# Kernel optimization log

Hardware: AMD Instinct MI355X
Metric: run time of the kernel (lower is better)

Reference implementation:

```python
import jax, jax.numpy as jnp
import numpy as np

B, S, D_IN, D_OUT = 4, 2048, 4096, 11008


def setup_inputs() -> dict:
    key = jax.random.key(0)
    k1, k2, k3, k4 = jax.random.split(key, 4)
    x = jax.random.normal(k1, (B, S, D_IN), dtype=jnp.float32)
    # quantized int8 codes (stored int32 per harness dtype set)
    weight_q = jax.random.randint(k2, (D_OUT, D_IN), 0, 127, dtype=jnp.int32)
    scale = jax.random.uniform(k3, (1,), dtype=jnp.float32) * 0.01 + 1e-4
    bias = jax.random.normal(k4, (D_OUT,), dtype=jnp.float32)
    return {"x": x, "weight_q": weight_q, "scale": scale, "bias": bias}


def reference(x, weight_q, scale, bias):
    # dequantize: int codes * per-tensor scale -> fp32 weight [D_OUT, D_IN]
    weight_fp = weight_q.astype(jnp.float32) * scale[0]
    # F.linear: y = x @ W^T + b
    return jnp.einsum('bsd,od->bso', x, weight_fp) + bias
```

## Files before the change

### kernel.cpp

```cpp
#include <hip/hip_runtime.h>
#include <hip/hip_bf16.h>
#include <stdint.h>

#define M_TOT 8192
#define N_TOT 11008
#define K_TOT 4096
#define BM 256
#define BN 256
#define BK 64
#define KT (K_TOT / BK)
#define NTM (M_TOT / BM)
#define NTN (N_TOT / BN)
#define NBLK (NTM * NTN)
#define BUFB 32768
#define LDSB (4 * BUFB)
#define ROWB K_TOT

typedef int i32x4 __attribute__((ext_vector_type(4)));

__global__ __launch_bounds__(256) void quant_x_kernel(const float* __restrict__ x,
                                                      char* __restrict__ xq,
                                                      float* __restrict__ sr) {
  __shared__ float red[4];
  const int r = blockIdx.x;
  const int t = threadIdx.x;
  const float4* px = (const float4*)(x + (long)r * K_TOT) + t * 4;
  float4 v0 = px[0], v1 = px[1], v2 = px[2], v3 = px[3];
  float f[16] = {v0.x, v0.y, v0.z, v0.w, v1.x, v1.y, v1.z, v1.w,
                 v2.x, v2.y, v2.z, v2.w, v3.x, v3.y, v3.z, v3.w};
  float m = 0.f;
#pragma unroll
  for (int i = 0; i < 16; ++i) m = fmaxf(m, fabsf(f[i]));
#pragma unroll
  for (int off = 1; off < 64; off <<= 1) m = fmaxf(m, __shfl_xor(m, off));
  if ((t & 63) == 0) red[t >> 6] = m;
  __syncthreads();
  m = fmaxf(fmaxf(red[0], red[1]), fmaxf(red[2], red[3]));
  m = fmaxf(m, 1e-20f);
  const float inv = 127.0f / m;
  int q[16];
#pragma unroll
  for (int i = 0; i < 16; ++i) q[i] = __float2int_rn(f[i] * inv);
  int4 o;
  o.x = (q[0] & 255) | ((q[1] & 255) << 8) | ((q[2] & 255) << 16) | (q[3] << 24);
  o.y = (q[4] & 255) | ((q[5] & 255) << 8) | ((q[6] & 255) << 16) | (q[7] << 24);
  o.z = (q[8] & 255) | ((q[9] & 255) << 8) | ((q[10] & 255) << 16) | (q[11] << 24);
  o.w = (q[12] & 255) | ((q[13] & 255) << 8) | ((q[14] & 255) << 16) | (q[15] << 24);
  ((int4*)(xq + (long)r * K_TOT))[t] = o;
  if (t == 0) sr[r] = m / 127.0f;
}

__global__ __launch_bounds__(256) void cvt_w8_kernel(const int* __restrict__ w,
                                                     char* __restrict__ wq,
                                                     long n16) {
  long i = (long)blockIdx.x * 256 + threadIdx.x;
  if (i >= n16) return;
  const int4* p = (const int4*)w + i * 4;
  int4 a = p[0], b = p[1], c = p[2], d = p[3];
  int4 o;
  o.x = (a.x & 255) | ((a.y & 255) << 8) | ((a.z & 255) << 16) | (a.w << 24);
  o.y = (b.x & 255) | ((b.y & 255) << 8) | ((b.z & 255) << 16) | (b.w << 24);
  o.z = (c.x & 255) | ((c.y & 255) << 8) | ((c.z & 255) << 16) | (c.w << 24);
  o.w = (d.x & 255) | ((d.y & 255) << 8) | ((d.z & 255) << 16) | (d.w << 24);
  ((int4*)wq)[i] = o;
}

__device__ __forceinline__ void gload_lds16(const void* g, void* l) {
  __builtin_amdgcn_global_load_lds((const __attribute__((address_space(1))) void*)g,
                                   (__attribute__((address_space(3))) void*)l,
                                   16, 0, 0);
}

__global__ __launch_bounds__(512, 2) void gemm256_i8_kernel(
    const unsigned char* __restrict__ A,
    const unsigned char* __restrict__ Bw,
    const float* __restrict__ sr,
    const float* __restrict__ scale,
    const float* __restrict__ bias,
    float* __restrict__ C) {
  extern __shared__ char lds[];
  const int tid = threadIdx.x;
  const int lane = tid & 63;
  const int wid = tid >> 6;
  const int wm = wid >> 2;
  const int wn = wid & 3;
  const int l16 = lane & 15;
  const int kh = lane >> 4;

  const int bid = blockIdx.x;
  const int wg = (bid & 7) * (NBLK / 8) + (bid >> 3);
  const int tm = wg / NTN, tn = wg % NTN;
  const long m0 = (long)tm * BM, n0 = (long)tn * BN;

  const int prl = tid >> 3;
  const int cp = ((tid & 7) * 16) ^ ((prl & 7) << 4);
  const int hsel = cp >> 6;
  const int colb = cp & 63;
  const char* gA = (const char*)A + (m0 + 2 * prl + hsel) * (long)ROWB + colb;
  const char* gB = (const char*)Bw + (n0 + 2 * prl + hsel) * (long)ROWB + colb;
  const int ldsT = tid * 16;

  const int inner = (((lane & 1) << 6) | (kh << 4)) ^ (((l16 >> 1) & 7) << 4);
  const int aB = (wm * 64 + (l16 >> 1)) * 128 + inner;
  const int bB = 16384 + (wn * 32 + (l16 >> 1)) * 128 + inner;

  i32x4 acc[8][4] = {};
  i32x4 afP[4], afN[4], bfA[4], bfB[4];

#define STG_A(q, kb) gload_lds16(gA + (q) * (128L * ROWB) + (kb), lds + sOff + (q) * 8192 + ldsT)
#define STG_B(q, kb) gload_lds16(gB + (q) * (128L * ROWB) + (kb), lds + sOff + 16384 + (q) * 8192 + ldsT)

  int sOff = 0;
  STG_A(0, 0); STG_A(1, 0); STG_B(0, 0); STG_B(1, 0);
  sOff = BUFB;
  STG_A(0, 64); STG_A(1, 64); STG_B(0, 64); STG_B(1, 64);
  sOff = 2 * BUFB;
  STG_A(0, 128); STG_A(1, 128); STG_B(0, 128); STG_B(1, 128);
  asm volatile("s_waitcnt vmcnt(8)" ::: "memory");
  asm volatile("s_barrier" ::: "memory");
#pragma unroll
  for (int i = 0; i < 4; ++i) {
    afP[i] = *(const i32x4*)(lds + aB + i * 1024);
    bfA[i] = *(const i32x4*)(lds + bB + i * 1024);
  }

  int cOff = 0;
  sOff = 3 * BUFB;
  long ktB = 3 * 64;
  int t = 0;

#define ITER(BF_CUR, BF_NXT)                                                  \
  {                                                                           \
    const char* La = lds + cOff;                                              \
    if (t < KT - 2) asm volatile("s_waitcnt vmcnt(4)" ::: "memory");          \
    else            asm volatile("s_waitcnt vmcnt(0)" ::: "memory");          \
    asm volatile("s_barrier" ::: "memory");                                   \
    if (t < KT - 3) { STG_A(0, ktB); STG_A(1, ktB); STG_B(0, ktB); STG_B(1, ktB); } \
    _Pragma("unroll")                                                         \
    for (int i = 0; i < 4; ++i)                                               \
      afN[i] = *(const i32x4*)(La + aB + 4096 + i * 1024);                    \
    __builtin_amdgcn_sched_barrier(0);                                        \
    __builtin_amdgcn_s_setprio(1);                                            \
    _Pragma("unroll")                                                         \
    for (int mi = 0; mi < 4; ++mi)                                            \
      _Pragma("unroll")                                                       \
      for (int ni = 0; ni < 4; ++ni)                                          \
        acc[mi][ni] = __builtin_amdgcn_mfma_i32_16x16x64_i8(afP[mi], BF_CUR[ni], acc[mi][ni], 0, 0, 0); \
    __builtin_amdgcn_s_setprio(0);                                            \
    __builtin_amdgcn_sched_barrier(0);                                        \
    if (t < KT - 1) {                                                         \
      const char* Ln = lds + ((cOff + BUFB) & (LDSB - 1));                    \
      _Pragma("unroll")                                                       \
      for (int i = 0; i < 4; ++i) {                                           \
        afP[i] = *(const i32x4*)(Ln + aB + i * 1024);                         \
        BF_NXT[i] = *(const i32x4*)(Ln + bB + i * 1024);                      \
      }                                                                       \
    }                                                                         \
    __builtin_amdgcn_sched_barrier(0);                                        \
    __builtin_amdgcn_s_setprio(1);                                            \
    _Pragma("unroll")                                                         \
    for (int mi = 0; mi < 4; ++mi)                                            \
      _Pragma("unroll")                                                       \
      for (int ni = 0; ni < 4; ++ni)                                          \
        acc[4 + mi][ni] = __builtin_amdgcn_mfma_i32_16x16x64_i8(afN[mi], BF_CUR[ni], acc[4 + mi][ni], 0, 0, 0); \
    __builtin_amdgcn_s_setprio(0);                                            \
    cOff = (cOff + BUFB) & (LDSB - 1);                                        \
    sOff = (sOff + BUFB) & (LDSB - 1);                                        \
    ktB += 64;                                                                \
    ++t;                                                                      \
  }

  for (int tt = 0; tt < KT / 2; ++tt) {
    ITER(bfA, bfB);
    ITER(bfB, bfA);
  }
#undef ITER
#undef STG_A
#undef STG_B

  const float sw = scale[0];
  float bv[4];
#pragma unroll
  for (int ni = 0; ni < 4; ++ni) bv[ni] = bias[n0 + wn * 64 + ni * 16 + l16];
#pragma unroll
  for (int mi = 0; mi < 8; ++mi) {
#pragma unroll
    for (int j = 0; j < 4; ++j) {
      const long row = m0 + wm * 128 + mi * 16 + kh * 4 + j;
      const float rsw = sr[row] * sw;
#pragma unroll
      for (int ni = 0; ni < 4; ++ni) {
        const long col = n0 + wn * 64 + ni * 16 + l16;
        C[row * N_TOT + col] = (float)acc[mi][ni][j] * rsw + bv[ni];
      }
    }
  }
}

__global__ __launch_bounds__(256) void naive_kernel(const float* __restrict__ x,
                                                    const int* __restrict__ wq,
                                                    const float* __restrict__ scale,
                                                    const float* __restrict__ bias,
                                                    float* __restrict__ out) {
  long idx = (long)blockIdx.x * 256 + threadIdx.x;
  if (idx >= (long)M_TOT * N_TOT) return;
  long m = idx / N_TOT, n = idx % N_TOT;
  const float* xr = x + m * (long)K_TOT;
  const int* wr = wq + n * (long)K_TOT;
  float acc = 0.f;
  for (int k = 0; k < K_TOT; ++k) acc += xr[k] * (float)wr[k];
  out[idx] = acc * scale[0] + bias[n];
}

extern "C" void kernel_launch(void* const* d_in, const int* in_sizes, int n_in,
                              void* d_out, int out_size, void* d_ws, size_t ws_size,
                              hipStream_t stream) {
  const float* x = (const float*)d_in[0];
  const int* wq = (const int*)d_in[1];
  const float* scale = (const float*)d_in[2];
  const float* bias = (const float*)d_in[3];
  float* out = (float*)d_out;

  const long xe = (long)M_TOT * K_TOT;
  const long we = (long)N_TOT * K_TOT;
  const size_t need = (size_t)xe + we + M_TOT * sizeof(float);

  if (ws_size >= need) {
    char* xq = (char*)d_ws;
    char* wb = xq + xe;
    float* sr = (float*)(wb + we);
    quant_x_kernel<<<M_TOT, 256, 0, stream>>>(x, xq, sr);
    cvt_w8_kernel<<<(int)((we / 16 + 255) / 256), 256, 0, stream>>>(wq, wb, we / 16);
    (void)hipFuncSetAttribute((const void*)gemm256_i8_kernel,
                              hipFuncAttributeMaxDynamicSharedMemorySize, LDSB);
    gemm256_i8_kernel<<<NBLK, 512, LDSB, stream>>>((const unsigned char*)xq,
                                                   (const unsigned char*)wb,
                                                   sr, scale, bias, out);
  } else {
    long total = (long)M_TOT * N_TOT;
    naive_kernel<<<(int)((total + 255) / 256), 256, 0, stream>>>(x, wq, scale, bias, out);
  }
}
```

Baseline: 463.2 us.

## Load A operand directly from global into registers, stage only B in LDS

The A tile no longer passes through LDS. Each wave now loads its A fragments straight from global memory into registers with inline global_load_dwordx4, and only the B tile is staged in LDS, which halves the LDS buffer size. This is meant to cut LDS traffic and LDS footprint, possibly allowing better occupancy. The cost is more global loads per wave and a more fragile vmcnt-based wait scheme, and the direct A loads may coalesce poorly and miss the reuse that LDS sharing across waves provided.

```diff
diff --git a/kernel.cpp b/kernel.cpp
--- a/kernel.cpp
+++ b/kernel.cpp
@@ -12,7 +12,7 @@
 #define NTM (M_TOT / BM)
 #define NTN (N_TOT / BN)
 #define NBLK (NTM * NTN)
-#define BUFB 32768
+#define BUFB 16384
 #define LDSB (4 * BUFB)
 #define ROWB K_TOT
 
@@ -70,6 +70,9 @@
                                    (__attribute__((address_space(3))) void*)l,
                                    16, 0, 0);
 }
+
+#define LDG(dst, p) \
+  asm volatile("global_load_dwordx4 %0, %1, off" : "=v"(dst) : "v"((const void*)(p)))
 
 __global__ __launch_bounds__(512, 2) void gemm256_i8_kernel(
     const unsigned char* __restrict__ A,
@@ -96,86 +99,86 @@
   const int cp = ((tid & 7) * 16) ^ ((prl & 7) << 4);
   const int hsel = cp >> 6;
   const int colb = cp & 63;
-  const char* gA = (const char*)A + (m0 + 2 * prl + hsel) * (long)ROWB + colb;
   const char* gB = (const char*)Bw + (n0 + 2 * prl + hsel) * (long)ROWB + colb;
   const int ldsT = tid * 16;
 
   const int inner = (((lane & 1) << 6) | (kh << 4)) ^ (((l16 >> 1) & 7) << 4);
-  const int aB = (wm * 64 + (l16 >> 1)) * 128 + inner;
-  const int bB = 16384 + (wn * 32 + (l16 >> 1)) * 128 + inner;
+  const int bB = (wn * 32 + (l16 >> 1)) * 128 + inner;
+
+  const char* aP = (const char*)A + (m0 + wm * 128 + l16) * (long)ROWB + kh * 16;
 
   i32x4 acc[8][4] = {};
-  i32x4 afP[4], afN[4], bfA[4], bfB[4];
-
-#define STG_A(q, kb) gload_lds16(gA + (q) * (128L * ROWB) + (kb), lds + sOff + (q) * 8192 + ldsT)
-#define STG_B(q, kb) gload_lds16(gB + (q) * (128L * ROWB) + (kb), lds + sOff + 16384 + (q) * 8192 + ldsT)
+  i32x4 aL0[4], aL1[4], aHi[4], bf[4];
+
+#define STG_B(q, kb) gload_lds16(gB + (q) * (128L * ROWB) + (kb), lds + sOff + (q) * 8192 + ldsT)
 
   int sOff = 0;
-  STG_A(0, 0); STG_A(1, 0); STG_B(0, 0); STG_B(1, 0);
+  STG_B(0, 0); STG_B(1, 0);
   sOff = BUFB;
-  STG_A(0, 64); STG_A(1, 64); STG_B(0, 64); STG_B(1, 64);
+  STG_B(0, 64); STG_B(1, 64);
   sOff = 2 * BUFB;
-  STG_A(0, 128); STG_A(1, 128); STG_B(0, 128); STG_B(1, 128);
-  asm volatile("s_waitcnt vmcnt(8)" ::: "memory");
+  STG_B(0, 128); STG_B(1, 128);
+#pragma unroll
+  for (int i = 0; i < 4; ++i) LDG(aL0[i], aP + i * (16L * ROWB));
+  __builtin_amdgcn_sched_barrier(0);
+  asm volatile("s_waitcnt vmcnt(0)" ::: "memory");
+  __builtin_amdgcn_sched_barrier(0);
   asm volatile("s_barrier" ::: "memory");
-#pragma unroll
-  for (int i = 0; i < 4; ++i) {
-    afP[i] = *(const i32x4*)(lds + aB + i * 1024);
-    bfA[i] = *(const i32x4*)(lds + bB + i * 1024);
-  }
 
   int cOff = 0;
   sOff = 3 * BUFB;
+  long ktA = 0;
   long ktB = 3 * 64;
   int t = 0;
 
-#define ITER(BF_CUR, BF_NXT)                                                  \
+#define ITER(ALC, ALN)                                                        \
   {                                                                           \
-    const char* La = lds + cOff;                                              \
-    if (t < KT - 2) asm volatile("s_waitcnt vmcnt(4)" ::: "memory");          \
+    asm volatile("s_barrier" ::: "memory");                 \
+    _Pragma("unroll")                                                         \
+    for (int ni = 0; ni < 4; ++ni)                                            \
+      bf[ni] = *(const i32x4*)(lds + cOff + bB + ni * 1024);                  \
+    _Pragma("unroll")                                                         \
+    for (int i = 0; i < 4; ++i) LDG(aHi[i], aP + (4 + i) * (16L * ROWB) + ktA); \
+    if (t < KT - 1) {                                                         \
+      _Pragma("unroll")                                                       \
+      for (int i = 0; i < 4; ++i) LDG(ALN[i], aP + i * (16L * ROWB) + ktA + 64); \
+    }                                                                         \
+    if (t < KT - 3) { STG_B(0, ktB); STG_B(1, ktB); }                         \
+    __builtin_amdgcn_sched_barrier(0);                                        \
+    if (t < KT - 3) asm volatile("s_waitcnt vmcnt(12)" ::: "memory");         \
     else            asm volatile("s_waitcnt vmcnt(0)" ::: "memory");          \
-    asm volatile("s_barrier" ::: "memory");                                   \
-    if (t < KT - 3) { STG_A(0, ktB); STG_A(1, ktB); STG_B(0, ktB); STG_B(1, ktB); } \
-    _Pragma("unroll")                                                         \
-    for (int i = 0; i < 4; ++i)                                               \
-      afN[i] = *(const i32x4*)(La + aB + 4096 + i * 1024);                    \
     __builtin_amdgcn_sched_barrier(0);                                        \
     __builtin_amdgcn_s_setprio(1);                                            \
     _Pragma("unroll")                                                         \
     for (int mi = 0; mi < 4; ++mi)                                            \
       _Pragma("unroll")                                                       \
       for (int ni = 0; ni < 4; ++ni)                                          \
-        acc[mi][ni] = __builtin_amdgcn_mfma_i32_16x16x64_i8(afP[mi], BF_CUR[ni], acc[mi][ni], 0, 0, 0); \
+        acc[mi][ni] = __builtin_amdgcn_mfma_i32_16x16x64_i8(ALC[mi], bf[ni], acc[mi][ni], 0, 0, 0); \
     __builtin_amdgcn_s_setprio(0);                                            \
     __builtin_amdgcn_sched_barrier(0);                                        \
-    if (t < KT - 1) {                                                         \
-      const char* Ln = lds + ((cOff + BUFB) & (LDSB - 1));                    \
-      _Pragma("unroll")                                                       \
-      for (int i = 0; i < 4; ++i) {                                           \
-        afP[i] = *(const i32x4*)(Ln + aB + i * 1024);                         \
-        BF_NXT[i] = *(const i32x4*)(Ln + bB + i * 1024);                      \
-      }                                                                       \
-    }                                                                         \
+    if (t < KT - 3) asm volatile("s_waitcnt vmcnt(6)" ::: "memory");          \
+    else            asm volatile("s_waitcnt vmcnt(0)" ::: "memory");          \
     __builtin_amdgcn_sched_barrier(0);                                        \
     __builtin_amdgcn_s_setprio(1);                                            \
     _Pragma("unroll")                                                         \
     for (int mi = 0; mi < 4; ++mi)                                            \
       _Pragma("unroll")                                                       \
       for (int ni = 0; ni < 4; ++ni)                                          \
-        acc[4 + mi][ni] = __builtin_amdgcn_mfma_i32_16x16x64_i8(afN[mi], BF_CUR[ni], acc[4 + mi][ni], 0, 0, 0); \
+        acc[4 + mi][ni] = __builtin_amdgcn_mfma_i32_16x16x64_i8(aHi[mi], bf[ni], acc[4 + mi][ni], 0, 0, 0); \
     __builtin_amdgcn_s_setprio(0);                                            \
+    __builtin_amdgcn_sched_barrier(0);                                        \
     cOff = (cOff + BUFB) & (LDSB - 1);                                        \
     sOff = (sOff + BUFB) & (LDSB - 1);                                        \
+    ktA += 64;                                                                \
     ktB += 64;                                                                \
     ++t;                                                                      \
   }
 
   for (int tt = 0; tt < KT / 2; ++tt) {
-    ITER(bfA, bfB);
-    ITER(bfB, bfA);
+    ITER(aL0, aL1);
+    ITER(aL1, aL0);
   }
 #undef ITER
-#undef STG_A
 #undef STG_B
 
   const float sw = scale[0];
```

Result: slower. 913.6 us (+97.2%).

## Shrink GEMM tile to 256x128 with four waves and a three-stage LDS ring

Applied to the files above, without the earlier changes.

The int8 GEMM block tile goes from 256x256 with 8 waves to 256x128 with 4 waves, so each wave keeps its 128x64 accumulator footprint. The LDS ring goes from four stages to three, with stage indices fixed at compile time through a 6-way unrolled loop. The wait and barrier now sit between the two MFMA halves instead of at the top of each iteration. This doubles the block count for better balance across CUs, but reloads more operand data per output, prefetches one stage less, and halves waves resident per CU.

```diff
diff --git a/kernel.cpp b/kernel.cpp
--- a/kernel.cpp
+++ b/kernel.cpp
@@ -6,14 +6,14 @@
 #define N_TOT 11008
 #define K_TOT 4096
 #define BM 256
-#define BN 256
+#define BN 128
 #define BK 64
 #define KT (K_TOT / BK)
 #define NTM (M_TOT / BM)
 #define NTN (N_TOT / BN)
 #define NBLK (NTM * NTN)
-#define BUFB 32768
-#define LDSB (4 * BUFB)
+#define BUFB 24576
+#define LDSB (3 * BUFB)
 #define ROWB K_TOT
 
 typedef int i32x4 __attribute__((ext_vector_type(4)));
@@ -71,7 +71,7 @@
                                    16, 0, 0);
 }
 
-__global__ __launch_bounds__(512, 2) void gemm256_i8_kernel(
+__global__ __launch_bounds__(256, 2) void gemm256_i8_kernel(
     const unsigned char* __restrict__ A,
     const unsigned char* __restrict__ Bw,
     const float* __restrict__ sr,
@@ -82,8 +82,8 @@
   const int tid = threadIdx.x;
   const int lane = tid & 63;
   const int wid = tid >> 6;
-  const int wm = wid >> 2;
-  const int wn = wid & 3;
+  const int wm = wid >> 1;
+  const int wn = wid & 1;
   const int l16 = lane & 15;
   const int kh = lane >> 4;
 
@@ -107,16 +107,16 @@
   i32x4 acc[8][4] = {};
   i32x4 afP[4], afN[4], bfA[4], bfB[4];
 
-#define STG_A(q, kb) gload_lds16(gA + (q) * (128L * ROWB) + (kb), lds + sOff + (q) * 8192 + ldsT)
-#define STG_B(q, kb) gload_lds16(gB + (q) * (128L * ROWB) + (kb), lds + sOff + 16384 + (q) * 8192 + ldsT)
-
-  int sOff = 0;
-  STG_A(0, 0); STG_A(1, 0); STG_B(0, 0); STG_B(1, 0);
-  sOff = BUFB;
-  STG_A(0, 64); STG_A(1, 64); STG_B(0, 64); STG_B(1, 64);
-  sOff = 2 * BUFB;
-  STG_A(0, 128); STG_A(1, 128); STG_B(0, 128); STG_B(1, 128);
-  asm volatile("s_waitcnt vmcnt(8)" ::: "memory");
+#define STG_A(S, q, kb) gload_lds16(gA + (q) * (64L * ROWB) + (kb), \
+                                    lds + (S) * BUFB + (q) * 4096 + ldsT)
+#define STG_B(S, q, kb) gload_lds16(gB + (q) * (64L * ROWB) + (kb), \
+                                    lds + (S) * BUFB + 16384 + (q) * 4096 + ldsT)
+
+  STG_A(0, 0, 0); STG_A(0, 1, 0); STG_A(0, 2, 0); STG_A(0, 3, 0);
+  STG_B(0, 0, 0); STG_B(0, 1, 0);
+  STG_A(1, 0, 64); STG_A(1, 1, 64); STG_A(1, 2, 64); STG_A(1, 3, 64);
+  STG_B(1, 0, 64); STG_B(1, 1, 64);
+  asm volatile("s_waitcnt vmcnt(6)" ::: "memory");
   asm volatile("s_barrier" ::: "memory");
 #pragma unroll
   for (int i = 0; i < 4; ++i) {
@@ -124,21 +124,20 @@
     bfA[i] = *(const i32x4*)(lds + bB + i * 1024);
   }
 
-  int cOff = 0;
-  sOff = 3 * BUFB;
-  long ktB = 3 * 64;
+  long ktB = 2 * 64;
   int t = 0;
 
-#define ITER(BF_CUR, BF_NXT)                                                  \
+#define ITER(SC, SN, SS, KOFF, BF_CUR, BF_NXT)                                \
   {                                                                           \
-    const char* La = lds + cOff;                                              \
-    if (t < KT - 2) asm volatile("s_waitcnt vmcnt(4)" ::: "memory");          \
-    else            asm volatile("s_waitcnt vmcnt(0)" ::: "memory");          \
-    asm volatile("s_barrier" ::: "memory");                                   \
-    if (t < KT - 3) { STG_A(0, ktB); STG_A(1, ktB); STG_B(0, ktB); STG_B(1, ktB); } \
+    asm volatile("s_barrier" ::: "memory");      \
+    if (t < KT - 2) {                                                         \
+      STG_A(SS, 0, ktB + KOFF); STG_A(SS, 1, ktB + KOFF);                     \
+      STG_A(SS, 2, ktB + KOFF); STG_A(SS, 3, ktB + KOFF);                     \
+      STG_B(SS, 0, ktB + KOFF); STG_B(SS, 1, ktB + KOFF);                     \
+    }                                                                         \
     _Pragma("unroll")                                                         \
     for (int i = 0; i < 4; ++i)                                               \
-      afN[i] = *(const i32x4*)(La + aB + 4096 + i * 1024);                    \
+      afN[i] = *(const i32x4*)(lds + (SC) * BUFB + aB + 4096 + i * 1024);     \
     __builtin_amdgcn_sched_barrier(0);                                        \
     __builtin_amdgcn_s_setprio(1);                                            \
     _Pragma("unroll")                                                         \
@@ -148,12 +147,14 @@
         acc[mi][ni] = __builtin_amdgcn_mfma_i32_16x16x64_i8(afP[mi], BF_CUR[ni], acc[mi][ni], 0, 0, 0); \
     __builtin_amdgcn_s_setprio(0);                                            \
     __builtin_amdgcn_sched_barrier(0);                                        \
+    if (t < KT - 2) asm volatile("s_waitcnt vmcnt(6)" ::: "memory");          \
+    else            asm volatile("s_waitcnt vmcnt(0)" ::: "memory");          \
+    asm volatile("s_barrier" ::: "memory");             \
     if (t < KT - 1) {                                                         \
-      const char* Ln = lds + ((cOff + BUFB) & (LDSB - 1));                    \
       _Pragma("unroll")                                                       \
       for (int i = 0; i < 4; ++i) {                                           \
-        afP[i] = *(const i32x4*)(Ln + aB + i * 1024);                         \
-        BF_NXT[i] = *(const i32x4*)(Ln + bB + i * 1024);                      \
+        afP[i] = *(const i32x4*)(lds + (SN) * BUFB + aB + i * 1024);          \
+        BF_NXT[i] = *(const i32x4*)(lds + (SN) * BUFB + bB + i * 1024);       \
       }                                                                       \
     }                                                                         \
     __builtin_amdgcn_sched_barrier(0);                                        \
@@ -164,16 +165,23 @@
       for (int ni = 0; ni < 4; ++ni)                                          \
         acc[4 + mi][ni] = __builtin_amdgcn_mfma_i32_16x16x64_i8(afN[mi], BF_CUR[ni], acc[4 + mi][ni], 0, 0, 0); \
     __builtin_amdgcn_s_setprio(0);                                            \
-    cOff = (cOff + BUFB) & (LDSB - 1);                                        \
-    sOff = (sOff + BUFB) & (LDSB - 1);                                        \
-    ktB += 64;                                                                \
+    __builtin_amdgcn_sched_barrier(0);                                        \
     ++t;                                                                      \
   }
 
-  for (int tt = 0; tt < KT / 2; ++tt) {
-    ITER(bfA, bfB);
-    ITER(bfB, bfA);
-  }
+  for (int tt = 0; tt < 10; ++tt) {
+    ITER(0, 1, 2, 0,   bfA, bfB);
+    ITER(1, 2, 0, 64,  bfB, bfA);
+    ITER(2, 0, 1, 128, bfA, bfB);
+    ITER(0, 1, 2, 192, bfB, bfA);
+    ITER(1, 2, 0, 256, bfA, bfB);
+    ITER(2, 0, 1, 320, bfB, bfA);
+    ktB += 384;
+  }
+  ITER(0, 1, 2, 0,   bfA, bfB);
+  ITER(1, 2, 0, 64,  bfB, bfA);
+  ITER(2, 0, 1, 128, bfA, bfB);
+  ITER(0, 1, 2, 192, bfB, bfA);
 #undef ITER
 #undef STG_A
 #undef STG_B
@@ -233,7 +241,7 @@
     cvt_w8_kernel<<<(int)((we / 16 + 255) / 256), 256, 0, stream>>>(wq, wb, we / 16);
     (void)hipFuncSetAttribute((const void*)gemm256_i8_kernel,
                               hipFuncAttributeMaxDynamicSharedMemorySize, LDSB);
-    gemm256_i8_kernel<<<NBLK, 512, LDSB, stream>>>((const unsigned char*)xq,
+    gemm256_i8_kernel<<<NBLK, 256, LDSB, stream>>>((const unsigned char*)xq,
                                                    (const unsigned char*)wb,
                                                    sr, scale, bias, out);
   } else {
```

New measurement: 468.4 us. No clear change (+1.1%).
